# Optimization experiments

Hardware: AMD Instinct MI355X
Metric: run time of the kernel (lower is better)

The kernel has to match this reference:

```python
import jax, jax.numpy as jnp
import numpy as np

N_NODES = 50000
N_EDGES = 800000
HID = 128
EDGE_FEAT = 4
NUM_G = 20
R_MIN, R_MAX = 0.0, 100.0  # r_max = 10.0**2


def _mlp2(x, w1, b1, w2, b2, act_last):
    y = jax.nn.relu(x @ w1 + b1)
    y = y @ w2 + b2
    return jax.nn.relu(y) if act_last else y


def _linear_init(key, fan_in, fan_out):
    kw, kb = jax.random.split(key)
    lim = 1.0 / np.sqrt(fan_in)
    w = jax.random.uniform(kw, (fan_in, fan_out), jnp.float32, -lim, lim)
    b = jax.random.uniform(kb, (fan_out,), jnp.float32, -lim, lim)
    return w, b


def setup_inputs():
    key = jax.random.key(0)
    ks = jax.random.split(key, 16)
    src = jax.random.randint(ks[0], (N_EDGES,), 0, N_NODES)
    dst = jax.random.randint(ks[1], (N_EDGES,), 0, N_NODES)
    edge_feat = jax.random.normal(ks[2], (N_EDGES, EDGE_FEAT), jnp.float32)
    h = jax.random.normal(ks[3], (N_NODES, HID), jnp.float32)
    x = jax.random.normal(ks[4], (N_NODES, 3), jnp.float32)
    ein = 2 * HID + EDGE_FEAT + NUM_G
    ew1, eb1 = _linear_init(ks[5], ein, HID)
    ew2, eb2 = _linear_init(ks[6], HID, HID)
    infw, infb = _linear_init(ks[7], HID, 1)
    xw1, xb1 = _linear_init(ks[8], HID, HID)
    xw2, xb2 = _linear_init(ks[9], HID, 1)
    nw1, nb1 = _linear_init(ks[10], 2 * HID, HID)
    nw2, nb2 = _linear_init(ks[11], HID, HID)
    return {"src": src, "dst": dst, "edge_feat": edge_feat, "h": h, "x": x,
            "ew1": ew1, "eb1": eb1, "ew2": ew2, "eb2": eb2,
            "infw": infw, "infb": infb,
            "xw1": xw1, "xb1": xb1, "xw2": xw2, "xb2": xb2,
            "nw1": nw1, "nb1": nb1, "nw2": nw2, "nb2": nb2}


def reference(src, dst, edge_feat, h, x,
              ew1, eb1, ew2, eb2, infw, infb,
              xw1, xb1, xw2, xb2, nw1, nb1, nw2, nb2):
    n_nodes = h.shape[0]
    rel_x = x[dst] - x[src]                      # [E, 3]
    r = jnp.sum(rel_x * rel_x, -1, keepdims=True)  # [E, 1]
    # GaussianSmearing expansion
    offsets = jnp.linspace(R_MIN, R_MAX, NUM_G)
    coeff = -0.5 / (offsets[1] - offsets[0]) ** 2
    r_feat = jnp.exp(coeff * (r - offsets) ** 2)  # [E, NUM_G]
    # edge message MLP (act_last=True)
    cat = jnp.concatenate([edge_feat, r_feat, h[dst], h[src]], axis=-1)
    mij = _mlp2(cat, ew1, eb1, ew2, eb2, act_last=True)  # [E, HID]
    eij = jax.nn.sigmoid(mij @ infw + infb)              # [E, 1]
    mi = jax.ops.segment_sum(mij * eij, dst, num_segments=n_nodes)  # [N, HID]
    h_new = h + _mlp2(jnp.concatenate([mi, h], -1), nw1, nb1, nw2, nb2, act_last=False)
    # coordinate update: (xi - xj) == rel_x
    x_scale = _mlp2(mij, xw1, xb1, xw2, xb2, act_last=False)  # [E, 1]
    delta_x = jax.ops.segment_sum(rel_x * x_scale, dst, num_segments=n_nodes)
    x_new = x + delta_x
    return h_new, x_new
```

## Files before the change

### kernel.cpp

```cpp
#include <hip/hip_runtime.h>

#define HID 128
#define NNODES 50000
#define NEDGES 800000

typedef __attribute__((ext_vector_type(8))) short short8;
typedef __attribute__((ext_vector_type(4))) float f32x4;

union U8 { short8 v; unsigned short u[8]; };

__device__ __forceinline__ unsigned short f2b(float f) {
  unsigned int u = __float_as_uint(f);
  u += 0x7FFFu + ((u >> 16) & 1u);
  return (unsigned short)(u >> 16);
}

__device__ __forceinline__ unsigned int pk2(float a, float b) {
  unsigned int ua = __float_as_uint(a);
  ua += 0x7FFFu + ((ua >> 16) & 1u);
  unsigned int ub = __float_as_uint(b);
  ub += 0x7FFFu + ((ub >> 16) & 1u);
  return (ua >> 16) | (ub & 0xFFFF0000u);
}

// ... 13 lines not shown

__global__ __launch_bounds__(256) void pack_kernel(
    const float* __restrict__ ew1, const float* __restrict__ ew2,
    const float* __restrict__ xw1, const float* __restrict__ nw1,
    const float* __restrict__ nw2, unsigned short* __restrict__ ws) {
  int i = blockIdx.x * 256 + threadIdx.x;
  const float* w; int base, ksrc;
  if (i < 36864)       { w = ew1; base = 0;      ksrc = 280; }
  else if (i < 53248)  { w = ew2; base = 36864;  ksrc = 128; }
  else if (i < 69632)  { w = xw1; base = 53248;  ksrc = 128; }
  else if (i < 102400) { w = nw1; base = 69632;  ksrc = 256; }
  else if (i < 118784) { w = nw2; base = 102400; ksrc = 128; }
  else return;
  int li = i - base;
  int j = li & 7, t = li >> 3;
  int col = t & 127, kg = t >> 7;
  int k = kg * 8 + j;
  float v = (k < ksrc) ? w[k * 128 + col] : 0.0f;
  ws[i] = f2b(v);
}

__global__ __launch_bounds__(256) void hpack_kernel(
    const float* __restrict__ h, unsigned short* __restrict__ hB) {
  int i = blockIdx.x * 256 + threadIdx.x;
  const float4* p = reinterpret_cast<const float4*>(h + (size_t)i * 8);
  float4 a = p[0], b = p[1];
  uint4 u;
  u.x = pk2(a.x, a.y); u.y = pk2(a.z, a.w);
  u.z = pk2(b.x, b.y); u.w = pk2(b.z, b.w);
  *reinterpret_cast<uint4*>(hB + (size_t)i * 8) = u;
}

template<int MODE>
__global__ __launch_bounds__(256, 4) void edge_kernel(
    const int* __restrict__ src, const int* __restrict__ dst,
    const float* __restrict__ ef, const float* __restrict__ h,
    const float* __restrict__ x,
    const float* __restrict__ eb1, const float* __restrict__ eb2,
    const float* __restrict__ infw, const float* __restrict__ infb,
    const float* __restrict__ xb1, const float* __restrict__ xw2,
    const float* __restrict__ xb2,
    const short8* __restrict__ W1p, const short8* __restrict__ W2p,
    const short8* __restrict__ XW1p,
    const unsigned short* __restrict__ hB,
    float* __restrict__ miF, unsigned short* __restrict__ miB,
    float* __restrict__ dx) {
  __shared__ __align__(16) char catB[64 * 576];
  __shared__ int dL[64], sL[64];
  __shared__ float relL[64][3];
  __shared__ float ppart[4][64];
  __shared__ float eijL[64];

  const int tid = threadIdx.x;
  const int e0 = blockIdx.x * 64;
  const int lane = tid & 63, w = tid >> 6;
  const int lr = lane & 15, lg = lane >> 4;
  const int l7 = lr & 7, l3 = lr & 3;
  const int colb = w*32 + lr;

  {
    int row = tid >> 2, sub = tid & 3;
    int e = e0 + row;
    int s = src[e], d = dst[e];
    if (sub == 0) { sL[row] = s; dL[row] = d; }
    float rx = x[3*d+0] - x[3*s+0];
    float ry = x[3*d+1] - x[3*s+1];
    float rz = x[3*d+2] - x[3*s+2];
    if (sub == 1) { relL[row][0] = rx; relL[row][1] = ry; relL[row][2] = rz; }
    float r = rx*rx + ry*ry + rz*rz;
    const float step = 100.0f / 19.0f;
    const float co = -0.5f / (step * step);
    float v6[6];
    if (sub == 0) {
      const float4 efv = reinterpret_cast<const float4*>(ef)[e];
      v6[0]=efv.x; v6[1]=efv.y; v6[2]=efv.z; v6[3]=efv.w;
      float t1 = r - step;
      v6[4] = __expf(co * r * r);
      v6[5] = __expf(co * t1 * t1);
    } else {
      #pragma unroll
      for (int q = 0; q < 6; ++q) {
        float g = (float)(sub*6 - 4 + q) * step;
        float t = r - g;
        v6[q] = __expf(co * t * t);
      }
    }
    #pragma unroll
    for (int q = 0; q < 3; ++q) {
      int c = sub*6 + q*2;
      int chunk = (c>>3) ^ (row&7);
      *reinterpret_cast<unsigned int*>(catB + row*576 + (chunk<<4) + ((c&7)<<1)) = pk2h(v6[q*2], v6[q*2+1]);
    }
    if (sub == 3) {
      U8 z;
      #pragma unroll
      for (int j = 0; j < 8; ++j) z.u[j] = 0;
      *reinterpret_cast<short8*>(catB + row*576 + ((32 + (3 ^ (row&3)))<<4)) = z.v;
    }
  }

  #pragma unroll
  for (int it = 0; it < 8; ++it) {
    int i = tid + it*256;
    int row = i >> 5, c = i & 31;
    int node = (c < 16) ? dst[e0+row] : src[e0+row];
    int chunk = 3 + c;
    int sw = (chunk < 32) ? (chunk ^ (row&7)) : (32 + ((chunk&3) ^ (row&3)));
    if (MODE == 2) {
      short8 u = *reinterpret_cast<const short8*>(hB + (size_t)node*128 + (c&15)*8);
      *reinterpret_cast<short8*>(catB + row*576 + (sw<<4)) = u;
    } else {
      const float4* hp = reinterpret_cast<const float4*>(h + (size_t)node*128 + (c&15)*8);
      float4 a = hp[0], b = hp[1];
      uint4 u;
      u.x = pk2(a.x, a.y); u.y = pk2(a.z, a.w);
      u.z = pk2(b.x, b.y); u.w = pk2(b.z, b.w);
      *reinterpret_cast<uint4*>(catB + row*576 + (sw<<4)) = u;
    }
  }

  short8 p00 = W1p[(0*4+lg)*128 + colb], p01 = W1p[(0*4+lg)*128 + colb + 16];
  short8 p10 = W1p[(1*4+lg)*128 + colb], p11 = W1p[(1*4+lg)*128 + colb + 16];
  __syncthreads();

  f32x4 acc[4][2];
  #pragma unroll
  for (int t = 0; t < 4; ++t) { acc[t][0] = (f32x4)0.0f; acc[t][1] = (f32x4)0.0f; }
  #pragma unroll
  for (int kt = 0; kt < 9; ++kt) {
    int ch = (kt < 8) ? ((kt*4+lg) ^ l7) : (32 + (lg ^ l3));
    short8 a0 = *reinterpret_cast<const short8*>(catB + (0*16+lr)*576 + (ch<<4));
    short8 a1 = *reinterpret_cast<const short8*>(catB + (1*16+lr)*576 + (ch<<4));
    short8 a2 = *reinterpret_cast<const short8*>(catB + (2*16+lr)*576 + (ch<<4));
    short8 a3 = *reinterpret_cast<const short8*>(catB + (3*16+lr)*576 + (ch<<4));
    short8 b0, b1;
    if (kt == 0)      { b0 = p00; b1 = p01; }
    else if (kt == 1) { b0 = p10; b1 = p11; }
    else              { b0 = W1p[(kt*4+lg)*128 + colb]; b1 = W1p[(kt*4+lg)*128 + colb + 16]; }
    acc[0][0] = __builtin_amdgcn_mfma_f32_16x16x32_bf16(b0, a0, acc[0][0], 0, 0, 0);
    acc[0][1] = __builtin_amdgcn_mfma_f32_16x16x32_bf16(b1, a0, acc[0][1], 0, 0, 0);
    acc[1][0] = __builtin_amdgcn_mfma_f32_16x16x32_bf16(b0, a1, acc[1][0], 0, 0, 0);
    acc[1][1] = __builtin_amdgcn_mfma_f32_16x16x32_bf16(b1, a1, acc[1][1], 0, 0, 0);
    acc[2][0] = __builtin_amdgcn_mfma_f32_16x16x32_bf16(b0, a2, acc[2][0], 0, 0, 0);
    acc[2][1] = __builtin_amdgcn_mfma_f32_16x16x32_bf16(b1, a2, acc[2][1], 0, 0, 0);
    acc[3][0] = __builtin_amdgcn_mfma_f32_16x16x32_bf16(b0, a3, acc[3][0], 0, 0, 0);
    acc[3][1] = __builtin_amdgcn_mfma_f32_16x16x32_bf16(b1, a3, acc[3][1], 0, 0, 0);
  }
  __syncthreads();

  {
    const int c00 = w*32 + lg*4, c01 = c00 + 16;
    float4 be0 = *reinterpret_cast<const float4*>(eb1 + c00);
    float4 be1 = *reinterpret_cast<const float4*>(eb1 + c01);
    #pragma unroll
    for (int t = 0; t < 4; ++t) {
      int row = t*16 + lr;
      char* rowB = catB + row*576;
      #pragma unroll
      for (int j = 0; j < 2; ++j) {
        const float4 be = j ? be1 : be0;
        int c0 = j ? c01 : c00;
        float v0 = fmaxf(acc[t][j][0] + be.x, 0.f);
        float v1 = fmaxf(acc[t][j][1] + be.y, 0.f);
        float v2 = fmaxf(acc[t][j][2] + be.z, 0.f);
        float v3 = fmaxf(acc[t][j][3] + be.w, 0.f);
        uint2 pv; pv.x = pk2h(v0, v1); pv.y = pk2h(v2, v3);
        int chunk = (c0>>3) ^ (row&7);
        *reinterpret_cast<uint2*>(rowB + (chunk<<4) + ((c0&7)<<1)) = pv;
      }
    }
  }
  __syncthreads();

  f32x4 acc2[4][2];
  #pragma unroll
  for (int t = 0; t < 4; ++t) { acc2[t][0] = (f32x4)0.0f; acc2[t][1] = (f32x4)0.0f; }
  #pragma unroll
  for (int kt = 0; kt < 4; ++kt) {
    int ch = (kt*4+lg) ^ l7;
    short8 a0 = *reinterpret_cast<const short8*>(catB + (0*16+lr)*576 + (ch<<4));
    short8 a1 = *reinterpret_cast<const short8*>(catB + (1*16+lr)*576 + (ch<<4));
    short8 a2 = *reinterpret_cast<const short8*>(catB + (2*16+lr)*576 + (ch<<4));
    short8 a3 = *reinterpret_cast<const short8*>(catB + (3*16+lr)*576 + (ch<<4));
    short8 b0 = W2p[(kt*4+lg)*128 + colb];
    short8 b1 = W2p[(kt*4+lg)*128 + colb + 16];
    acc2[0][0] = __builtin_amdgcn_mfma_f32_16x16x32_bf16(b0, a0, acc2[0][0], 0, 0, 0);
    acc2[0][1] = __builtin_amdgcn_mfma_f32_16x16x32_bf16(b1, a0, acc2[0][1], 0, 0, 0);
    acc2[1][0] = __builtin_amdgcn_mfma_f32_16x16x32_bf16(b0, a1, acc2[1][0], 0, 0, 0);
    acc2[1][1] = __builtin_amdgcn_mfma_f32_16x16x32_bf16(b1, a1, acc2[1][1], 0, 0, 0);
    acc2[2][0] = __builtin_amdgcn_mfma_f32_16x16x32_bf16(b0, a2, acc2[2][0], 0, 0, 0);
    acc2[2][1] = __builtin_amdgcn_mfma_f32_16x16x32_bf16(b1, a2, acc2[2][1], 0, 0, 0);
    acc2[3][0] = __builtin_amdgcn_mfma_f32_16x16x32_bf16(b0, a3, acc2[3][0], 0, 0, 0);
    acc2[3][1] = __builtin_amdgcn_mfma_f32_16x16x32_bf16(b1, a3, acc2[3][1], 0, 0, 0);
  }
  float pl[4];
  {
    const int c00 = w*32 + lg*4, c01 = c00 + 16;
    float4 be0 = *reinterpret_cast<const float4*>(eb2 + c00);
    float4 be1 = *reinterpret_cast<const float4*>(eb2 + c01);
    float4 iw0 = *reinterpret_cast<const float4*>(infw + c00);
    float4 iw1 = *reinterpret_cast<const float4*>(infw + c01);
    #pragma unroll
    for (int t = 0; t < 4; ++t) {
      int row = t*16 + lr;
      char* rowB = catB + row*576;
      pl[t] = 0.f;
      #pragma unroll
      for (int j = 0; j < 2; ++j) {
        const float4 be = j ? be1 : be0;
        const float4 iw = j ? iw1 : iw0;
        int c0 = j ? c01 : c00;
        float v0 = fmaxf(acc2[t][j][0] + be.x, 0.f);
        float v1 = fmaxf(acc2[t][j][1] + be.y, 0.f);
        float v2 = fmaxf(acc2[t][j][2] + be.z, 0.f);
        float v3 = fmaxf(acc2[t][j][3] + be.w, 0.f);
        acc2[t][j][0] = v0; acc2[t][j][1] = v1; acc2[t][j][2] = v2; acc2[t][j][3] = v3;
        pl[t] += v0*iw.x + v1*iw.y + v2*iw.z + v3*iw.w;
        uint2 pv; pv.x = pk2h(v0, v1); pv.y = pk2h(v2, v3);
        int chunk = 16 + ((c0>>3) ^ (row&7));
        *reinterpret_cast<uint2*>(rowB + (chunk<<4) + ((c0&7)<<1)) = pv;
      }
    }
    #pragma unroll
    for (int t = 0; t < 4; ++t) {
      pl[t] += __shfl_xor(pl[t], 16, 64);
      pl[t] += __shfl_xor(pl[t], 32, 64);
    }
    if (lane < 16) {
      #pragma unroll
      for (int t = 0; t < 4; ++t) ppart[w][t*16 + lane] = pl[t];
    }
  }
  __syncthreads();

  if (lane < 16) {
    int row2 = w*16 + lane;
    float s2 = ppart[0][row2] + ppart[1][row2] + ppart[2][row2] + ppart[3][row2] + infb[0];
    eijL[row2] = 1.f / (1.f + __expf(-s2));
  }
  __syncthreads();

  if (MODE >= 1) {
    const int c00 = w*32 + lg*4, c01 = c00 + 16;
    #pragma unroll
    for (int t = 0; t < 4; ++t) {
      int row = t*16 + lr;
      float e = eijL[row];
      char* rowB = catB + row*576;
      #pragma unroll
      for (int j = 0; j < 2; ++j) {
        int c0 = j ? c01 : c00;
        uint2 pv;
        pv.x = pk2h(acc2[t][j][0]*e, acc2[t][j][1]*e);
        pv.y = pk2h(acc2[t][j][2]*e, acc2[t][j][3]*e);
        *reinterpret_cast<uint2*>(rowB + (stage_chunk(c0, row)<<4) + ((c0&7)<<1)) = pv;
      }
    }
  } else {
    const int c00 = w*32 + lg*4, c01 = c00 + 16;
    #pragma unroll
    for (int t = 0; t < 4; ++t) {
      int row = t*16 + lr;
      int d = dL[row];
      float e = eijL[row];
      float* fp = miF + (size_t)d*128;
      #pragma unroll
      for (int j = 0; j < 2; ++j) {
        int c0 = j ? c01 : c00;
        #pragma unroll
        for (int rg = 0; rg < 4; ++rg) atomicAdd(fp + c0 + rg, acc2[t][j][rg]*e);
      }
    }
  }
  __syncthreads();

  if (MODE >= 1) {
    #pragma unroll
    for (int t = 0; t < 4; ++t)
      #pragma unroll
      for (int rg = 0; rg < 4; ++rg) {
        int row = t*16 + lg*4 + rg;
        int d = dL[row];
        int col0 = w*32 + lr*2;
        unsigned int val = *reinterpret_cast<const unsigned int*>(
            catB + row*576 + (stage_chunk(col0, row)<<4) + ((col0&7)<<1));
        if (val) atomicPkAddBf16(miB + (size_t)d*128 + col0, val);
      }
  }

  f32x4 acc3[4][2];
  #pragma unroll
  for (int t = 0; t < 4; ++t) { acc3[t][0] = (f32x4)0.0f; acc3[t][1] = (f32x4)0.0f; }
  #pragma unroll
  for (int kt = 0; kt < 4; ++kt) {
    int ch = 16 + ((kt*4+lg) ^ l7);
    short8 a0 = *reinterpret_cast<const short8*>(catB + (0*16+lr)*576 + (ch<<4));
    short8 a1 = *reinterpret_cast<const short8*>(catB + (1*16+lr)*576 + (ch<<4));
    short8 a2 = *reinterpret_cast<const short8*>(catB + (2*16+lr)*576 + (ch<<4));
    short8 a3 = *reinterpret_cast<const short8*>(catB + (3*16+lr)*576 + (ch<<4));
    short8 b0 = XW1p[(kt*4+lg)*128 + colb];
    short8 b1 = XW1p[(kt*4+lg)*128 + colb + 16];
    acc3[0][0] = __builtin_amdgcn_mfma_f32_16x16x32_bf16(b0, a0, acc3[0][0], 0, 0, 0);
    acc3[0][1] = __builtin_amdgcn_mfma_f32_16x16x32_bf16(b1, a0, acc3[0][1], 0, 0, 0);
    acc3[1][0] = __builtin_amdgcn_mfma_f32_16x16x32_bf16(b0, a1, acc3[1][0], 0, 0, 0);
    acc3[1][1] = __builtin_amdgcn_mfma_f32_16x16x32_bf16(b1, a1, acc3[1][1], 0, 0, 0);
    acc3[2][0] = __builtin_amdgcn_mfma_f32_16x16x32_bf16(b0, a2, acc3[2][0], 0, 0, 0);
    acc3[2][1] = __builtin_amdgcn_mfma_f32_16x16x32_bf16(b1, a2, acc3[2][1], 0, 0, 0);
    acc3[3][0] = __builtin_amdgcn_mfma_f32_16x16x32_bf16(b0, a3, acc3[3][0], 0, 0, 0);
    acc3[3][1] = __builtin_amdgcn_mfma_f32_16x16x32_bf16(b1, a3, acc3[3][1], 0, 0, 0);
  }

  {
    const int c00 = w*32 + lg*4, c01 = c00 + 16;
    float4 bx0 = *reinterpret_cast<const float4*>(xb1 + c00);
    float4 bx1 = *reinterpret_cast<const float4*>(xb1 + c01);
    float4 xw0 = *reinterpret_cast<const float4*>(xw2 + c00);
    float4 xw1v = *reinterpret_cast<const float4*>(xw2 + c01);
    float ql[4];
    #pragma unroll
    for (int t = 0; t < 4; ++t) {
      ql[t] = 0.f;
      #pragma unroll
      for (int j = 0; j < 2; ++j) {
        const float4 bx = j ? bx1 : bx0;
        const float4 xw = j ? xw1v : xw0;
        ql[t] += fmaxf(acc3[t][j][0] + bx.x, 0.f) * xw.x
               + fmaxf(acc3[t][j][1] + bx.y, 0.f) * xw.y
               + fmaxf(acc3[t][j][2] + bx.z, 0.f) * xw.z
               + fmaxf(acc3[t][j][3] + bx.w, 0.f) * xw.w;
      }
      ql[t] += __shfl_xor(ql[t], 16, 64);
      ql[t] += __shfl_xor(ql[t], 32, 64);
    }
    if (lane < 16) {
      #pragma unroll
      for (int t = 0; t < 4; ++t) ppart[w][t*16 + lane] = ql[t];
    }
  }
  __syncthreads();

  if (tid < 192) {
    int row = tid / 3, c = tid - row*3;
    float q = ppart[0][row] + ppart[1][row] + ppart[2][row] + ppart[3][row] + xb2[0];
    atomicAdd(dx + dL[row]*3 + c, relL[row][c] * q);
  }
}

template<int MODE>
__global__ __launch_bounds__(256) void node_kernel(
    const float* __restrict__ h, const float* __restrict__ x,
    const float* __restrict__ nb1, const float* __restrict__ nb2,
    const short8* __restrict__ NW1p, const short8* __restrict__ NW2p,
    const unsigned short* __restrict__ miB,
    const unsigned short* __restrict__ hB,
    float* __restrict__ out) {
  __shared__ __align__(16) char c2B[64 * 512];
  __shared__ __align__(16) char y3B[64 * 256];
  const int tid = threadIdx.x;
  const int n0 = blockIdx.x * 64;
  const float* mi = out;

  for (int i = tid; i < 64*32; i += 256) {
    int row = i >> 5, c = i & 31;
    int node = n0 + row;
    U8 u;
    if (node < NNODES) {
      if (c < 16 && MODE >= 1) {
        u.v = *reinterpret_cast<const short8*>(miB + (size_t)node*128 + c*8);
      } else if (c >= 16 && MODE == 2) {
        u.v = *reinterpret_cast<const short8*>(hB + (size_t)node*128 + (c-16)*8);
      } else {
        const float4* p = (c < 16)
          ? reinterpret_cast<const float4*>(mi + (size_t)node*128 + c*8)
          : reinterpret_cast<const float4*>(h + (size_t)node*128 + (c-16)*8);
        float4 a = p[0], b = p[1];
        uint4 uu;
// ... 92 lines not shown
  const float* infb = (const float*)d_in[10];
  const float* xw1  = (const float*)d_in[11];
  const float* xb1  = (const float*)d_in[12];
  const float* xw2  = (const float*)d_in[13];
  const float* xb2  = (const float*)d_in[14];
  const float* nw1  = (const float*)d_in[15];
  const float* nb1  = (const float*)d_in[16];
  const float* nw2  = (const float*)d_in[17];
  const float* nb2  = (const float*)d_in[18];

  float* out = (float*)d_out;
  float* miF = out;
  float* dxp = out + NNODES*HID;
  unsigned short* wsp = (unsigned short*)d_ws;
  unsigned short* miB = wsp + 118784;
  unsigned short* hBp = miB + (size_t)NNODES*HID;

  const size_t MIN = (size_t)NNODES*HID;
  size_t need1 = (118784u + MIN) * 2u;
  size_t need2 = (118784u + 2u*MIN) * 2u;
  int mode = (ws_size >= need2) ? 2 : (ws_size >= need1 ? 1 : 0);

  if (mode >= 1) {
    hipMemsetAsync(miB, 0, MIN*2, stream);
    hipMemsetAsync(dxp, 0, (size_t)NNODES*3*4, stream);
  } else {
    hipMemsetAsync(d_out, 0, (size_t)out_size * sizeof(float), stream);
  }

  pack_kernel<<<464, 256, 0, stream>>>(ew1, ew2, xw1, nw1, nw2, wsp);
  if (mode == 2) hpack_kernel<<<(NNODES*HID)/(256*8), 256, 0, stream>>>(h, hBp);

  if (mode == 2) {
    edge_kernel<2><<<NEDGES/64, 256, 0, stream>>>(
        src, dst, ef, h, x, eb1, eb2, infw, infb, xb1, xw2, xb2,
        (const short8*)wsp, (const short8*)(wsp + 36864), (const short8*)(wsp + 53248),
        hBp, miF, miB, dxp);
    node_kernel<2><<<(NNODES + 63)/64, 256, 0, stream>>>(
        h, x, nb1, nb2,
        (const short8*)(wsp + 69632), (const short8*)(wsp + 102400), miB, hBp, out);
  } else if (mode == 1) {
    edge_kernel<1><<<NEDGES/64, 256, 0, stream>>>(
        src, dst, ef, h, x, eb1, eb2, infw, infb, xb1, xw2, xb2,
        (const short8*)wsp, (const short8*)(wsp + 36864), (const short8*)(wsp + 53248),
        hBp, miF, miB, dxp);
    node_kernel<1><<<(NNODES + 63)/64, 256, 0, stream>>>(
        h, x, nb1, nb2,
        (const short8*)(wsp + 69632), (const short8*)(wsp + 102400), miB, hBp, out);
  } else {
    edge_kernel<0><<<NEDGES/64, 256, 0, stream>>>(
        src, dst, ef, h, x, eb1, eb2, infw, infb, xb1, xw2, xb2,
        (const short8*)wsp, (const short8*)(wsp + 36864), (const short8*)(wsp + 53248),
        hBp, miF, miB, dxp);
    node_kernel<0><<<(NNODES + 63)/64, 256, 0, stream>>>(
        h, x, nb1, nb2,
        (const short8*)(wsp + 69632), (const short8*)(wsp + 102400), miB, hBp, out);
  }
}
```

Before: 314.4 us.

## Split edge kernel work across 8 waves with 16 output columns each

Measured after the change: 458.5 us. 1.46x slower.

```diff
diff --git a/kernel.cpp b/kernel.cpp
--- a/kernel.cpp
+++ b/kernel.cpp
@@ -69,7 +69,7 @@
 }
 
 template<int MODE>
-__global__ __launch_bounds__(256, 4) void edge_kernel(
+__global__ __launch_bounds__(512, 8) void edge_kernel(
     const int* __restrict__ src, const int* __restrict__ dst,
     const float* __restrict__ ef, const float* __restrict__ h,
     const float* __restrict__ x,
@@ -85,7 +85,7 @@
   __shared__ __align__(16) char catB[64 * 576];
   __shared__ int dL[64], sL[64];
   __shared__ float relL[64][3];
-  __shared__ float ppart[4][64];
+  __shared__ float ppart[8][64];
   __shared__ float eijL[64];
 
   const int tid = threadIdx.x;
@@ -93,10 +93,11 @@
   const int lane = tid & 63, w = tid >> 6;
   const int lr = lane & 15, lg = lane >> 4;
   const int l7 = lr & 7, l3 = lr & 3;
-  const int colb = w*32 + lr;
+  const int colb = w*16 + lr;
+  const int c00 = w*16 + lg*4;
 
   {
-    int row = tid >> 2, sub = tid & 3;
+    int row = tid >> 3, sub = tid & 7;
     int e = e0 + row;
     int s = src[e], d = dst[e];
     if (sub == 0) { sL[row] = s; dL[row] = d; }
@@ -107,28 +108,24 @@
     float r = rx*rx + ry*ry + rz*rz;
     const float step = 100.0f / 19.0f;
     const float co = -0.5f / (step * step);
-    float v6[6];
-    if (sub == 0) {
-      const float4 efv = reinterpret_cast<const float4*>(ef)[e];
-      v6[0]=efv.x; v6[1]=efv.y; v6[2]=efv.z; v6[3]=efv.w;
-      float t1 = r - step;
-      v6[4] = __expf(co * r * r);
-      v6[5] = __expf(co * t1 * t1);
-    } else {
-      #pragma unroll
-      for (int q = 0; q < 6; ++q) {
-        float g = (float)(sub*6 - 4 + q) * step;
-        float t = r - g;
-        v6[q] = __expf(co * t * t);
+    if (sub < 6) {
+      float v4[4];
+      if (sub == 0) {
+        const float4 efv = reinterpret_cast<const float4*>(ef)[e];
+        v4[0]=efv.x; v4[1]=efv.y; v4[2]=efv.z; v4[3]=efv.w;
+      } else {
+        #pragma unroll
+        for (int q = 0; q < 4; ++q) {
+          float g = (float)(sub*4 - 4 + q) * step;
+          float t = r - g;
+          v4[q] = __expf(co * t * t);
+        }
       }
-    }
-    #pragma unroll
-    for (int q = 0; q < 3; ++q) {
-      int c = sub*6 + q*2;
+      int c = sub*4;
       int chunk = (c>>3) ^ (row&7);
-      *reinterpret_cast<unsigned int*>(catB + row*576 + (chunk<<4) + ((c&7)<<1)) = pk2h(v6[q*2], v6[q*2+1]);
-    }
-    if (sub == 3) {
+      uint2 pv; pv.x = pk2h(v4[0], v4[1]); pv.y = pk2h(v4[2], v4[3]);
+      *reinterpret_cast<uint2*>(catB + row*576 + (chunk<<4) + ((c&7)<<1)) = pv;
+    } else if (sub == 6) {
       U8 z;
       #pragma unroll
       for (int j = 0; j < 8; ++j) z.u[j] = 0;
@@ -137,8 +134,8 @@
   }
 
   #pragma unroll
-  for (int it = 0; it < 8; ++it) {
-    int i = tid + it*256;
+  for (int it = 0; it < 4; ++it) {
+    int i = tid + it*512;
     int row = i >> 5, c = i & 31;
     int node = (c < 16) ? dst[e0+row] : src[e0+row];
     int chunk = 3 + c;
@@ -156,13 +153,13 @@
     }
   }
 
-  short8 p00 = W1p[(0*4+lg)*128 + colb], p01 = W1p[(0*4+lg)*128 + colb + 16];
-  short8 p10 = W1p[(1*4+lg)*128 + colb], p11 = W1p[(1*4+lg)*128 + colb + 16];
-  __syncthreads();
-
-  f32x4 acc[4][2];
-  #pragma unroll
-  for (int t = 0; t < 4; ++t) { acc[t][0] = (f32x4)0.0f; acc[t][1] = (f32x4)0.0f; }
+  short8 p00 = W1p[(0*4+lg)*128 + colb];
+  short8 p10 = W1p[(1*4+lg)*128 + colb];
+  __syncthreads();
+
+  f32x4 acc[4];
+  #pragma unroll
+  for (int t = 0; t < 4; ++t) acc[t] = (f32x4)0.0f;
   #pragma unroll
   for (int kt = 0; kt < 9; ++kt) {
     int ch = (kt < 8) ? ((kt*4+lg) ^ l7) : (32 + (lg ^ l3));
@@ -170,48 +167,33 @@
     short8 a1 = *reinterpret_cast<const short8*>(catB + (1*16+lr)*576 + (ch<<4));
     short8 a2 = *reinterpret_cast<const short8*>(catB + (2*16+lr)*576 + (ch<<4));
     short8 a3 = *reinterpret_cast<const short8*>(catB + (3*16+lr)*576 + (ch<<4));
-    short8 b0, b1;
-    if (kt == 0)      { b0 = p00; b1 = p01; }
-    else if (kt == 1) { b0 = p10; b1 = p11; }
-    else              { b0 = W1p[(kt*4+lg)*128 + colb]; b1 = W1p[(kt*4+lg)*128 + colb + 16]; }
-    acc[0][0] = __builtin_amdgcn_mfma_f32_16x16x32_bf16(b0, a0, acc[0][0], 0, 0, 0);
-    acc[0][1] = __builtin_amdgcn_mfma_f32_16x16x32_bf16(b1, a0, acc[0][1], 0, 0, 0);
-    acc[1][0] = __builtin_amdgcn_mfma_f32_16x16x32_bf16(b0, a1, acc[1][0], 0, 0, 0);
-    acc[1][1] = __builtin_amdgcn_mfma_f32_16x16x32_bf16(b1, a1, acc[1][1], 0, 0, 0);
-    acc[2][0] = __builtin_amdgcn_mfma_f32_16x16x32_bf16(b0, a2, acc[2][0], 0, 0, 0);
-    acc[2][1] = __builtin_amdgcn_mfma_f32_16x16x32_bf16(b1, a2, acc[2][1], 0, 0, 0);
-    acc[3][0] = __builtin_amdgcn_mfma_f32_16x16x32_bf16(b0, a3, acc[3][0], 0, 0, 0);
-    acc[3][1] = __builtin_amdgcn_mfma_f32_16x16x32_bf16(b1, a3, acc[3][1], 0, 0, 0);
+    short8 b0 = (kt == 0) ? p00 : (kt == 1) ? p10 : W1p[(kt*4+lg)*128 + colb];
+    acc[0] = __builtin_amdgcn_mfma_f32_16x16x32_bf16(b0, a0, acc[0], 0, 0, 0);
+    acc[1] = __builtin_amdgcn_mfma_f32_16x16x32_bf16(b0, a1, acc[1], 0, 0, 0);
+    acc[2] = __builtin_amdgcn_mfma_f32_16x16x32_bf16(b0, a2, acc[2], 0, 0, 0);
+    acc[3] = __builtin_amdgcn_mfma_f32_16x16x32_bf16(b0, a3, acc[3], 0, 0, 0);
   }
   __syncthreads();
 
   {
-    const int c00 = w*32 + lg*4, c01 = c00 + 16;
-    float4 be0 = *reinterpret_cast<const float4*>(eb1 + c00);
-    float4 be1 = *reinterpret_cast<const float4*>(eb1 + c01);
+    float4 be = *reinterpret_cast<const float4*>(eb1 + c00);
     #pragma unroll
     for (int t = 0; t < 4; ++t) {
       int row = t*16 + lr;
-      char* rowB = catB + row*576;
-      #pragma unroll
-      for (int j = 0; j < 2; ++j) {
-        const float4 be = j ? be1 : be0;
-        int c0 = j ? c01 : c00;
-        float v0 = fmaxf(acc[t][j][0] + be.x, 0.f);
-        float v1 = fmaxf(acc[t][j][1] + be.y, 0.f);
-        float v2 = fmaxf(acc[t][j][2] + be.z, 0.f);
-        float v3 = fmaxf(acc[t][j][3] + be.w, 0.f);
-        uint2 pv; pv.x = pk2h(v0, v1); pv.y = pk2h(v2, v3);
-        int chunk = (c0>>3) ^ (row&7);
-        *reinterpret_cast<uint2*>(rowB + (chunk<<4) + ((c0&7)<<1)) = pv;
-      }
-    }
-  }
-  __syncthreads();
-
-  f32x4 acc2[4][2];
-  #pragma unroll
-  for (int t = 0; t < 4; ++t) { acc2[t][0] = (f32x4)0.0f; acc2[t][1] = (f32x4)0.0f; }
+      float v0 = fmaxf(acc[t][0] + be.x, 0.f);
+      float v1 = fmaxf(acc[t][1] + be.y, 0.f);
+      float v2 = fmaxf(acc[t][2] + be.z, 0.f);
+      float v3 = fmaxf(acc[t][3] + be.w, 0.f);
+      uint2 pv; pv.x = pk2h(v0, v1); pv.y = pk2h(v2, v3);
+      int chunk = (c00>>3) ^ (row&7);
+      *reinterpret_cast<uint2*>(catB + row*576 + (chunk<<4) + ((c00&7)<<1)) = pv;
+    }
+  }
+  __syncthreads();
+
+  f32x4 acc2[4];
+  #pragma unroll
+  for (int t = 0; t < 4; ++t) acc2[t] = (f32x4)0.0f;
   #pragma unroll
   for (int kt = 0; kt < 4; ++kt) {
     int ch = (kt*4+lg) ^ l7;
@@ -220,43 +202,27 @@
     short8 a2 = *reinterpret_cast<const short8*>(catB + (2*16+lr)*576 + (ch<<4));
     short8 a3 = *reinterpret_cast<const short8*>(catB + (3*16+lr)*576 + (ch<<4));
     short8 b0 = W2p[(kt*4+lg)*128 + colb];
-    short8 b1 = W2p[(kt*4+lg)*128 + colb + 16];
-    acc2[0][0] = __builtin_amdgcn_mfma_f32_16x16x32_bf16(b0, a0, acc2[0][0], 0, 0, 0);
-    acc2[0][1] = __builtin_amdgcn_mfma_f32_16x16x32_bf16(b1, a0, acc2[0][1], 0, 0, 0);
-    acc2[1][0] = __builtin_amdgcn_mfma_f32_16x16x32_bf16(b0, a1, acc2[1][0], 0, 0, 0);
-    acc2[1][1] = __builtin_amdgcn_mfma_f32_16x16x32_bf16(b1, a1, acc2[1][1], 0, 0, 0);
-    acc2[2][0] = __builtin_amdgcn_mfma_f32_16x16x32_bf16(b0, a2, acc2[2][0], 0, 0, 0);
-    acc2[2][1] = __builtin_amdgcn_mfma_f32_16x16x32_bf16(b1, a2, acc2[2][1], 0, 0, 0);
-    acc2[3][0] = __builtin_amdgcn_mfma_f32_16x16x32_bf16(b0, a3, acc2[3][0], 0, 0, 0);
-    acc2[3][1] = __builtin_amdgcn_mfma_f32_16x16x32_bf16(b1, a3, acc2[3][1], 0, 0, 0);
-  }
-  float pl[4];
+    acc2[0] = __builtin_amdgcn_mfma_f32_16x16x32_bf16(b0, a0, acc2[0], 0, 0, 0);
+    acc2[1] = __builtin_amdgcn_mfma_f32_16x16x32_bf16(b0, a1, acc2[1], 0, 0, 0);
+    acc2[2] = __builtin_amdgcn_mfma_f32_16x16x32_bf16(b0, a2, acc2[2], 0, 0, 0);
+    acc2[3] = __builtin_amdgcn_mfma_f32_16x16x32_bf16(b0, a3, acc2[3], 0, 0, 0);
+  }
   {
-    const int c00 = w*32 + lg*4, c01 = c00 + 16;
-    float4 be0 = *reinterpret_cast<const float4*>(eb2 + c00);
-    float4 be1 = *reinterpret_cast<const float4*>(eb2 + c01);
-    float4 iw0 = *reinterpret_cast<const float4*>(infw + c00);
-    float4 iw1 = *reinterpret_cast<const float4*>(infw + c01);
+    float4 be = *reinterpret_cast<const float4*>(eb2 + c00);
+    float4 iw = *reinterpret_cast<const float4*>(infw + c00);
+    float pl[4];
     #pragma unroll
     for (int t = 0; t < 4; ++t) {
       int row = t*16 + lr;
-      char* rowB = catB + row*576;
-      pl[t] = 0.f;
-      #pragma unroll
-      for (int j = 0; j < 2; ++j) {
-        const float4 be = j ? be1 : be0;
-        const float4 iw = j ? iw1 : iw0;
-        int c0 = j ? c01 : c00;
-        float v0 = fmaxf(acc2[t][j][0] + be.x, 0.f);
-        float v1 = fmaxf(acc2[t][j][1] + be.y, 0.f);
-        float v2 = fmaxf(acc2[t][j][2] + be.z, 0.f);
-        float v3 = fmaxf(acc2[t][j][3] + be.w, 0.f);
-        acc2[t][j][0] = v0; acc2[t][j][1] = v1; acc2[t][j][2] = v2; acc2[t][j][3] = v3;
-        pl[t] += v0*iw.x + v1*iw.y + v2*iw.z + v3*iw.w;
-        uint2 pv; pv.x = pk2h(v0, v1); pv.y = pk2h(v2, v3);
-        int chunk = 16 + ((c0>>3) ^ (row&7));
-        *reinterpret_cast<uint2*>(rowB + (chunk<<4) + ((c0&7)<<1)) = pv;
-      }
+      float v0 = fmaxf(acc2[t][0] + be.x, 0.f);
+      float v1 = fmaxf(acc2[t][1] + be.y, 0.f);
+      float v2 = fmaxf(acc2[t][2] + be.z, 0.f);
+      float v3 = fmaxf(acc2[t][3] + be.w, 0.f);
+      acc2[t][0]=v0; acc2[t][1]=v1; acc2[t][2]=v2; acc2[t][3]=v3;
+      pl[t] = v0*iw.x + v1*iw.y + v2*iw.z + v3*iw.w;
+      uint2 pv; pv.x = pk2h(v0, v1); pv.y = pk2h(v2, v3);
+      int chunk = 16 + ((c00>>3) ^ (row&7));
+      *reinterpret_cast<uint2*>(catB + row*576 + (chunk<<4) + ((c00&7)<<1)) = pv;
     }
     #pragma unroll
     for (int t = 0; t < 4; ++t) {
@@ -270,31 +236,25 @@
   }
   __syncthreads();
 
-  if (lane < 16) {
-    int row2 = w*16 + lane;
-    float s2 = ppart[0][row2] + ppart[1][row2] + ppart[2][row2] + ppart[3][row2] + infb[0];
-    eijL[row2] = 1.f / (1.f + __expf(-s2));
+  if (tid < 64) {
+    float s2 = infb[0];
+    #pragma unroll
+    for (int ww = 0; ww < 8; ++ww) s2 += ppart[ww][tid];
+    eijL[tid] = 1.f / (1.f + __expf(-s2));
   }
   __syncthreads();
 
   if (MODE >= 1) {
-    const int c00 = w*32 + lg*4, c01 = c00 + 16;
     #pragma unroll
     for (int t = 0; t < 4; ++t) {
       int row = t*16 + lr;
       float e = eijL[row];
-      char* rowB = catB + row*576;
-      #pragma unroll
-      for (int j = 0; j < 2; ++j) {
-        int c0 = j ? c01 : c00;
-        uint2 pv;
-        pv.x = pk2h(acc2[t][j][0]*e, acc2[t][j][1]*e);
-        pv.y = pk2h(acc2[t][j][2]*e, acc2[t][j][3]*e);
-        *reinterpret_cast<uint2*>(rowB + (stage_chunk(c0, row)<<4) + ((c0&7)<<1)) = pv;
-      }
+      uint2 pv;
+      pv.x = pk2h(acc2[t][0]*e, acc2[t][1]*e);
+      pv.y = pk2h(acc2[t][2]*e, acc2[t][3]*e);
+      *reinterpret_cast<uint2*>(catB + row*576 + (stage_chunk(c00, row)<<4) + ((c00&7)<<1)) = pv;
     }
   } else {
-    const int c00 = w*32 + lg*4, c01 = c00 + 16;
     #pragma unroll
     for (int t = 0; t < 4; ++t) {
       int row = t*16 + lr;
@@ -302,32 +262,27 @@
       float e = eijL[row];
       float* fp = miF + (size_t)d*128;
       #pragma unroll
-      for (int j = 0; j < 2; ++j) {
-        int c0 = j ? c01 : c00;
-        #pragma unroll
-        for (int rg = 0; rg < 4; ++rg) atomicAdd(fp + c0 + rg, acc2[t][j][rg]*e);
-      }
+      for (int rg = 0; rg < 4; ++rg) atomicAdd(fp + c00 + rg, acc2[t][rg]*e);
     }
   }
   __syncthreads();
 
   if (MODE >= 1) {
-    #pragma unroll
-    for (int t = 0; t < 4; ++t)
-      #pragma unroll
-      for (int rg = 0; rg < 4; ++rg) {
-        int row = t*16 + lg*4 + rg;
-        int d = dL[row];
-        int col0 = w*32 + lr*2;
-        unsigned int val = *reinterpret_cast<const unsigned int*>(
-            catB + row*576 + (stage_chunk(col0, row)<<4) + ((col0&7)<<1));
-        if (val) atomicPkAddBf16(miB + (size_t)d*128 + col0, val);
-      }
-  }
-
-  f32x4 acc3[4][2];
-  #pragma unroll
-  for (int t = 0; t < 4; ++t) { acc3[t][0] = (f32x4)0.0f; acc3[t][1] = (f32x4)0.0f; }
+    int col0 = w*16 + (lr & 7)*2;
+    int rsel = lg*2 + (lr >> 3);
+    #pragma unroll
+    for (int t2 = 0; t2 < 8; ++t2) {
+      int row = t2*8 + rsel;
+      int d = dL[row];
+      unsigned int val = *reinterpret_cast<const unsigned int*>(
+          catB + row*576 + (stage_chunk(col0, row)<<4) + ((col0&7)<<1));
+      if (val) atomicPkAddBf16(miB + (size_t)d*128 + col0, val);
+    }
+  }
+
+  f32x4 acc3[4];
+  #pragma unroll
+  for (int t = 0; t < 4; ++t) acc3[t] = (f32x4)0.0f;
   #pragma unroll
   for (int kt = 0; kt < 4; ++kt) {
     int ch = 16 + ((kt*4+lg) ^ l7);
@@ -336,36 +291,21 @@
     short8 a2 = *reinterpret_cast<const short8*>(catB + (2*16+lr)*576 + (ch<<4));
     short8 a3 = *reinterpret_cast<const short8*>(catB + (3*16+lr)*576 + (ch<<4));
     short8 b0 = XW1p[(kt*4+lg)*128 + colb];
-    short8 b1 = XW1p[(kt*4+lg)*128 + colb + 16];
-    acc3[0][0] = __builtin_amdgcn_mfma_f32_16x16x32_bf16(b0, a0, acc3[0][0], 0, 0, 0);
-    acc3[0][1] = __builtin_amdgcn_mfma_f32_16x16x32_bf16(b1, a0, acc3[0][1], 0, 0, 0);
-    acc3[1][0] = __builtin_amdgcn_mfma_f32_16x16x32_bf16(b0, a1, acc3[1][0], 0, 0, 0);
-    acc3[1][1] = __builtin_amdgcn_mfma_f32_16x16x32_bf16(b1, a1, acc3[1][1], 0, 0, 0);
-    acc3[2][0] = __builtin_amdgcn_mfma_f32_16x16x32_bf16(b0, a2, acc3[2][0], 0, 0, 0);
-    acc3[2][1] = __builtin_amdgcn_mfma_f32_16x16x32_bf16(b1, a2, acc3[2][1], 0, 0, 0);
-    acc3[3][0] = __builtin_amdgcn_mfma_f32_16x16x32_bf16(b0, a3, acc3[3][0], 0, 0, 0);
-    acc3[3][1] = __builtin_amdgcn_mfma_f32_16x16x32_bf16(b1, a3, acc3[3][1], 0, 0, 0);
-  }
-
+    acc3[0] = __builtin_amdgcn_mfma_f32_16x16x32_bf16(b0, a0, acc3[0], 0, 0, 0);
+    acc3[1] = __builtin_amdgcn_mfma_f32_16x16x32_bf16(b0, a1, acc3[1], 0, 0, 0);
+    acc3[2] = __builtin_amdgcn_mfma_f32_16x16x32_bf16(b0, a2, acc3[2], 0, 0, 0);
+    acc3[3] = __builtin_amdgcn_mfma_f32_16x16x32_bf16(b0, a3, acc3[3], 0, 0, 0);
+  }
   {
-    const int c00 = w*32 + lg*4, c01 = c00 + 16;
-    float4 bx0 = *reinterpret_cast<const float4*>(xb1 + c00);
-    float4 bx1 = *reinterpret_cast<const float4*>(xb1 + c01);
-    float4 xw0 = *reinterpret_cast<const float4*>(xw2 + c00);
-    float4 xw1v = *reinterpret_cast<const float4*>(xw2 + c01);
+    float4 bx = *reinterpret_cast<const float4*>(xb1 + c00);
+    float4 xw = *reinterpret_cast<const float4*>(xw2 + c00);
     float ql[4];
     #pragma unroll
     for (int t = 0; t < 4; ++t) {
-      ql[t] = 0.f;
-      #pragma unroll
-      for (int j = 0; j < 2; ++j) {
-        const float4 bx = j ? bx1 : bx0;
-        const float4 xw = j ? xw1v : xw0;
-        ql[t] += fmaxf(acc3[t][j][0] + bx.x, 0.f) * xw.x
-               + fmaxf(acc3[t][j][1] + bx.y, 0.f) * xw.y
-               + fmaxf(acc3[t][j][2] + bx.z, 0.f) * xw.z
-               + fmaxf(acc3[t][j][3] + bx.w, 0.f) * xw.w;
-      }
+      ql[t] = fmaxf(acc3[t][0] + bx.x, 0.f) * xw.x
+            + fmaxf(acc3[t][1] + bx.y, 0.f) * xw.y
+            + fmaxf(acc3[t][2] + bx.z, 0.f) * xw.z
+            + fmaxf(acc3[t][3] + bx.w, 0.f) * xw.w;
       ql[t] += __shfl_xor(ql[t], 16, 64);
       ql[t] += __shfl_xor(ql[t], 32, 64);
     }
@@ -378,7 +318,9 @@
 
   if (tid < 192) {
     int row = tid / 3, c = tid - row*3;
-    float q = ppart[0][row] + ppart[1][row] + ppart[2][row] + ppart[3][row] + xb2[0];
+    float q = xb2[0];
+    #pragma unroll
+    for (int ww = 0; ww < 8; ++ww) q += ppart[ww][row];
     atomicAdd(dx + dL[row]*3 + c, relL[row][c] * q);
   }
 }
@@ -537,7 +479,7 @@
   if (mode == 2) hpack_kernel<<<(NNODES*HID)/(256*8), 256, 0, stream>>>(h, hBp);
 
   if (mode == 2) {
-    edge_kernel<2><<<NEDGES/64, 256, 0, stream>>>(
+    edge_kernel<2><<<NEDGES/64, 512, 0, stream>>>(
         src, dst, ef, h, x, eb1, eb2, infw, infb, xb1, xw2, xb2,
         (const short8*)wsp, (const short8*)(wsp + 36864), (const short8*)(wsp + 53248),
         hBp, miF, miB, dxp);
@@ -545,7 +487,7 @@
         h, x, nb1, nb2,
         (const short8*)(wsp + 69632), (const short8*)(wsp + 102400), miB, hBp, out);
   } else if (mode == 1) {
-    edge_kernel<1><<<NEDGES/64, 256, 0, stream>>>(
+    edge_kernel<1><<<NEDGES/64, 512, 0, stream>>>(
         src, dst, ef, h, x, eb1, eb2, infw, infb, xb1, xw2, xb2,
         (const short8*)wsp, (const short8*)(wsp + 36864), (const short8*)(wsp + 53248),
         hBp, miF, miB, dxp);
@@ -553,7 +495,7 @@
         h, x, nb1, nb2,
         (const short8*)(wsp + 69632), (const short8*)(wsp + 102400), miB, hBp, out);
   } else {
-    edge_kernel<0><<<NEDGES/64, 256, 0, stream>>>(
+    edge_kernel<0><<<NEDGES/64, 512, 0, stream>>>(
         src, dst, ef, h, x, eb1, eb2, infw, infb, xb1, xw2, xb2,
         (const short8*)wsp, (const short8*)(wsp + 36864), (const short8*)(wsp + 53248),
         hBp, miF, miB, dxp);
```

## Split edge kernel work across 8 waves with 2x4 row/column wave tiling

Applied to the files above, without the earlier changes.

New measurement: 313.1 us (median of 2 runs). About the same (-0.4%).

```diff
diff --git a/kernel.cpp b/kernel.cpp
--- a/kernel.cpp
+++ b/kernel.cpp
@@ -69,7 +69,7 @@
 }
 
 template<int MODE>
-__global__ __launch_bounds__(256, 4) void edge_kernel(
+__global__ __launch_bounds__(512, 8) void edge_kernel(
     const int* __restrict__ src, const int* __restrict__ dst,
     const float* __restrict__ ef, const float* __restrict__ h,
     const float* __restrict__ x,
@@ -85,18 +85,21 @@
   __shared__ __align__(16) char catB[64 * 576];
   __shared__ int dL[64], sL[64];
   __shared__ float relL[64][3];
-  __shared__ float ppart[4][64];
+  __shared__ float ppart[8][64];
   __shared__ float eijL[64];
 
   const int tid = threadIdx.x;
   const int e0 = blockIdx.x * 64;
   const int lane = tid & 63, w = tid >> 6;
+  const int wm = w >> 2, wn = w & 3;
   const int lr = lane & 15, lg = lane >> 4;
   const int l7 = lr & 7, l3 = lr & 3;
-  const int colb = w*32 + lr;
+  const int colb = wn*32 + lr;
+  const int c00 = wn*32 + lg*4, c01 = c00 + 16;
+  const int rbase = wm*32;
 
   {
-    int row = tid >> 2, sub = tid & 3;
+    int row = tid >> 3, sub = tid & 7;
     int e = e0 + row;
     int s = src[e], d = dst[e];
     if (sub == 0) { sL[row] = s; dL[row] = d; }
@@ -107,28 +110,24 @@
     float r = rx*rx + ry*ry + rz*rz;
     const float step = 100.0f / 19.0f;
     const float co = -0.5f / (step * step);
-    float v6[6];
-    if (sub == 0) {
-      const float4 efv = reinterpret_cast<const float4*>(ef)[e];
-      v6[0]=efv.x; v6[1]=efv.y; v6[2]=efv.z; v6[3]=efv.w;
-      float t1 = r - step;
-      v6[4] = __expf(co * r * r);
-      v6[5] = __expf(co * t1 * t1);
-    } else {
-      #pragma unroll
-      for (int q = 0; q < 6; ++q) {
-        float g = (float)(sub*6 - 4 + q) * step;
-        float t = r - g;
-        v6[q] = __expf(co * t * t);
-      }
-    }
-    #pragma unroll
-    for (int q = 0; q < 3; ++q) {
-      int c = sub*6 + q*2;
+    if (sub < 6) {
+      float v4[4];
+      if (sub == 0) {
+        const float4 efv = reinterpret_cast<const float4*>(ef)[e];
+        v4[0]=efv.x; v4[1]=efv.y; v4[2]=efv.z; v4[3]=efv.w;
+      } else {
+        #pragma unroll
+        for (int q = 0; q < 4; ++q) {
+          float g = (float)(sub*4 - 4 + q) * step;
+          float t = r - g;
+          v4[q] = __expf(co * t * t);
+        }
+      }
+      int c = sub*4;
       int chunk = (c>>3) ^ (row&7);
-      *reinterpret_cast<unsigned int*>(catB + row*576 + (chunk<<4) + ((c&7)<<1)) = pk2h(v6[q*2], v6[q*2+1]);
-    }
-    if (sub == 3) {
+      uint2 pv; pv.x = pk2h(v4[0], v4[1]); pv.y = pk2h(v4[2], v4[3]);
+      *reinterpret_cast<uint2*>(catB + row*576 + (chunk<<4) + ((c&7)<<1)) = pv;
+    } else if (sub == 6) {
       U8 z;
       #pragma unroll
       for (int j = 0; j < 8; ++j) z.u[j] = 0;
@@ -137,8 +136,8 @@
   }
 
   #pragma unroll
-  for (int it = 0; it < 8; ++it) {
-    int i = tid + it*256;
+  for (int it = 0; it < 4; ++it) {
+    int i = tid + it*512;
     int row = i >> 5, c = i & 31;
     int node = (c < 16) ? dst[e0+row] : src[e0+row];
     int chunk = 3 + c;
@@ -160,16 +159,14 @@
   short8 p10 = W1p[(1*4+lg)*128 + colb], p11 = W1p[(1*4+lg)*128 + colb + 16];
   __syncthreads();
 
-  f32x4 acc[4][2];
-  #pragma unroll
-  for (int t = 0; t < 4; ++t) { acc[t][0] = (f32x4)0.0f; acc[t][1] = (f32x4)0.0f; }
+  f32x4 acc[2][2];
+  #pragma unroll
+  for (int t = 0; t < 2; ++t) { acc[t][0] = (f32x4)0.0f; acc[t][1] = (f32x4)0.0f; }
   #pragma unroll
   for (int kt = 0; kt < 9; ++kt) {
     int ch = (kt < 8) ? ((kt*4+lg) ^ l7) : (32 + (lg ^ l3));
-    short8 a0 = *reinterpret_cast<const short8*>(catB + (0*16+lr)*576 + (ch<<4));
-    short8 a1 = *reinterpret_cast<const short8*>(catB + (1*16+lr)*576 + (ch<<4));
-    short8 a2 = *reinterpret_cast<const short8*>(catB + (2*16+lr)*576 + (ch<<4));
-    short8 a3 = *reinterpret_cast<const short8*>(catB + (3*16+lr)*576 + (ch<<4));
+    short8 a0 = *reinterpret_cast<const short8*>(catB + (rbase + 0*16 + lr)*576 + (ch<<4));
+    short8 a1 = *reinterpret_cast<const short8*>(catB + (rbase + 1*16 + lr)*576 + (ch<<4));
     short8 b0, b1;
     if (kt == 0)      { b0 = p00; b1 = p01; }
     else if (kt == 1) { b0 = p10; b1 = p11; }
@@ -178,20 +175,15 @@
     acc[0][1] = __builtin_amdgcn_mfma_f32_16x16x32_bf16(b1, a0, acc[0][1], 0, 0, 0);
     acc[1][0] = __builtin_amdgcn_mfma_f32_16x16x32_bf16(b0, a1, acc[1][0], 0, 0, 0);
     acc[1][1] = __builtin_amdgcn_mfma_f32_16x16x32_bf16(b1, a1, acc[1][1], 0, 0, 0);
-    acc[2][0] = __builtin_amdgcn_mfma_f32_16x16x32_bf16(b0, a2, acc[2][0], 0, 0, 0);
-    acc[2][1] = __builtin_amdgcn_mfma_f32_16x16x32_bf16(b1, a2, acc[2][1], 0, 0, 0);
-    acc[3][0] = __builtin_amdgcn_mfma_f32_16x16x32_bf16(b0, a3, acc[3][0], 0, 0, 0);
-    acc[3][1] = __builtin_amdgcn_mfma_f32_16x16x32_bf16(b1, a3, acc[3][1], 0, 0, 0);
   }
   __syncthreads();
 
   {
-    const int c00 = w*32 + lg*4, c01 = c00 + 16;
     float4 be0 = *reinterpret_cast<const float4*>(eb1 + c00);
     float4 be1 = *reinterpret_cast<const float4*>(eb1 + c01);
     #pragma unroll
-    for (int t = 0; t < 4; ++t) {
-      int row = t*16 + lr;
+    for (int t = 0; t < 2; ++t) {
+      int row = rbase + t*16 + lr;
       char* rowB = catB + row*576;
       #pragma unroll
       for (int j = 0; j < 2; ++j) {
@@ -209,37 +201,30 @@
   }
   __syncthreads();
 
-  f32x4 acc2[4][2];
-  #pragma unroll
-  for (int t = 0; t < 4; ++t) { acc2[t][0] = (f32x4)0.0f; acc2[t][1] = (f32x4)0.0f; }
+  f32x4 acc2[2][2];
+  #pragma unroll
+  for (int t = 0; t < 2; ++t) { acc2[t][0] = (f32x4)0.0f; acc2[t][1] = (f32x4)0.0f; }
   #pragma unroll
   for (int kt = 0; kt < 4; ++kt) {
     int ch = (kt*4+lg) ^ l7;
-    short8 a0 = *reinterpret_cast<const short8*>(catB + (0*16+lr)*576 + (ch<<4));
-    short8 a1 = *reinterpret_cast<const short8*>(catB + (1*16+lr)*576 + (ch<<4));
-    short8 a2 = *reinterpret_cast<const short8*>(catB + (2*16+lr)*576 + (ch<<4));
-    short8 a3 = *reinterpret_cast<const short8*>(catB + (3*16+lr)*576 + (ch<<4));
+    short8 a0 = *reinterpret_cast<const short8*>(catB + (rbase + 0*16 + lr)*576 + (ch<<4));
+    short8 a1 = *reinterpret_cast<const short8*>(catB + (rbase + 1*16 + lr)*576 + (ch<<4));
     short8 b0 = W2p[(kt*4+lg)*128 + colb];
     short8 b1 = W2p[(kt*4+lg)*128 + colb + 16];
     acc2[0][0] = __builtin_amdgcn_mfma_f32_16x16x32_bf16(b0, a0, acc2[0][0], 0, 0, 0);
     acc2[0][1] = __builtin_amdgcn_mfma_f32_16x16x32_bf16(b1, a0, acc2[0][1], 0, 0, 0);
     acc2[1][0] = __builtin_amdgcn_mfma_f32_16x16x32_bf16(b0, a1, acc2[1][0], 0, 0, 0);
     acc2[1][1] = __builtin_amdgcn_mfma_f32_16x16x32_bf16(b1, a1, acc2[1][1], 0, 0, 0);
-    acc2[2][0] = __builtin_amdgcn_mfma_f32_16x16x32_bf16(b0, a2, acc2[2][0], 0, 0, 0);
-    acc2[2][1] = __builtin_amdgcn_mfma_f32_16x16x32_bf16(b1, a2, acc2[2][1], 0, 0, 0);
-    acc2[3][0] = __builtin_amdgcn_mfma_f32_16x16x32_bf16(b0, a3, acc2[3][0], 0, 0, 0);
-    acc2[3][1] = __builtin_amdgcn_mfma_f32_16x16x32_bf16(b1, a3, acc2[3][1], 0, 0, 0);
-  }
-  float pl[4];
+  }
   {
-    const int c00 = w*32 + lg*4, c01 = c00 + 16;
     float4 be0 = *reinterpret_cast<const float4*>(eb2 + c00);
     float4 be1 = *reinterpret_cast<const float4*>(eb2 + c01);
     float4 iw0 = *reinterpret_cast<const float4*>(infw + c00);
     float4 iw1 = *reinterpret_cast<const float4*>(infw + c01);
-    #pragma unroll
-    for (int t = 0; t < 4; ++t) {
-      int row = t*16 + lr;
+    float pl[2];
+    #pragma unroll
+    for (int t = 0; t < 2; ++t) {
+      int row = rbase + t*16 + lr;
       char* rowB = catB + row*576;
       pl[t] = 0.f;
       #pragma unroll
@@ -251,7 +236,7 @@
         float v1 = fmaxf(acc2[t][j][1] + be.y, 0.f);
         float v2 = fmaxf(acc2[t][j][2] + be.z, 0.f);
         float v3 = fmaxf(acc2[t][j][3] + be.w, 0.f);
-        acc2[t][j][0] = v0; acc2[t][j][1] = v1; acc2[t][j][2] = v2; acc2[t][j][3] = v3;
+        acc2[t][j][0]=v0; acc2[t][j][1]=v1; acc2[t][j][2]=v2; acc2[t][j][3]=v3;
         pl[t] += v0*iw.x + v1*iw.y + v2*iw.z + v3*iw.w;
         uint2 pv; pv.x = pk2h(v0, v1); pv.y = pk2h(v2, v3);
         int chunk = 16 + ((c0>>3) ^ (row&7));
@@ -259,29 +244,29 @@
       }
     }
     #pragma unroll
-    for (int t = 0; t < 4; ++t) {
+    for (int t = 0; t < 2; ++t) {
       pl[t] += __shfl_xor(pl[t], 16, 64);
       pl[t] += __shfl_xor(pl[t], 32, 64);
     }
     if (lane < 16) {
       #pragma unroll
-      for (int t = 0; t < 4; ++t) ppart[w][t*16 + lane] = pl[t];
-    }
-  }
-  __syncthreads();
-
-  if (lane < 16) {
-    int row2 = w*16 + lane;
-    float s2 = ppart[0][row2] + ppart[1][row2] + ppart[2][row2] + ppart[3][row2] + infb[0];
-    eijL[row2] = 1.f / (1.f + __expf(-s2));
+      for (int t = 0; t < 2; ++t) ppart[w][rbase + t*16 + lane] = pl[t];
+    }
+  }
+  __syncthreads();
+
+  if (tid < 64) {
+    int wmr = tid >> 5;
+    float s2 = infb[0] + ppart[wmr*4+0][tid] + ppart[wmr*4+1][tid]
+                       + ppart[wmr*4+2][tid] + ppart[wmr*4+3][tid];
+    eijL[tid] = 1.f / (1.f + __expf(-s2));
   }
   __syncthreads();
 
   if (MODE >= 1) {
-    const int c00 = w*32 + lg*4, c01 = c00 + 16;
-    #pragma unroll
-    for (int t = 0; t < 4; ++t) {
-      int row = t*16 + lr;
+    #pragma unroll
+    for (int t = 0; t < 2; ++t) {
+      int row = rbase + t*16 + lr;
       float e = eijL[row];
       char* rowB = catB + row*576;
       #pragma unroll
@@ -294,10 +279,9 @@
       }
     }
   } else {
-    const int c00 = w*32 + lg*4, c01 = c00 + 16;
-    #pragma unroll
-    for (int t = 0; t < 4; ++t) {
-      int row = t*16 + lr;
+    #pragma unroll
+    for (int t = 0; t < 2; ++t) {
+      int row = rbase + t*16 + lr;
       int d = dL[row];
       float e = eijL[row];
       float* fp = miF + (size_t)d*128;
@@ -312,50 +296,40 @@
   __syncthreads();
 
   if (MODE >= 1) {
-    #pragma unroll
-    for (int t = 0; t < 4; ++t)
-      #pragma unroll
-      for (int rg = 0; rg < 4; ++rg) {
-        int row = t*16 + lg*4 + rg;
-        int d = dL[row];
-        int col0 = w*32 + lr*2;
-        unsigned int val = *reinterpret_cast<const unsigned int*>(
-            catB + row*576 + (stage_chunk(col0, row)<<4) + ((col0&7)<<1));
-        if (val) atomicPkAddBf16(miB + (size_t)d*128 + col0, val);
-      }
-  }
-
-  f32x4 acc3[4][2];
-  #pragma unroll
-  for (int t = 0; t < 4; ++t) { acc3[t][0] = (f32x4)0.0f; acc3[t][1] = (f32x4)0.0f; }
+    int col0 = wn*32 + lr*2;
+    #pragma unroll
+    for (int t2 = 0; t2 < 8; ++t2) {
+      int row = rbase + t2*4 + lg;
+      int d = dL[row];
+      unsigned int val = *reinterpret_cast<const unsigned int*>(
+          catB + row*576 + (stage_chunk(col0, row)<<4) + ((col0&7)<<1));
+      if (val) atomicPkAddBf16(miB + (size_t)d*128 + col0, val);
+    }
+  }
+
+  f32x4 acc3[2][2];
+  #pragma unroll
+  for (int t = 0; t < 2; ++t) { acc3[t][0] = (f32x4)0.0f; acc3[t][1] = (f32x4)0.0f; }
   #pragma unroll
   for (int kt = 0; kt < 4; ++kt) {
     int ch = 16 + ((kt*4+lg) ^ l7);
-    short8 a0 = *reinterpret_cast<const short8*>(catB + (0*16+lr)*576 + (ch<<4));
-    short8 a1 = *reinterpret_cast<const short8*>(catB + (1*16+lr)*576 + (ch<<4));
-    short8 a2 = *reinterpret_cast<const short8*>(catB + (2*16+lr)*576 + (ch<<4));
-    short8 a3 = *reinterpret_cast<const short8*>(catB + (3*16+lr)*576 + (ch<<4));
+    short8 a0 = *reinterpret_cast<const short8*>(catB + (rbase + 0*16 + lr)*576 + (ch<<4));
+    short8 a1 = *reinterpret_cast<const short8*>(catB + (rbase + 1*16 + lr)*576 + (ch<<4));
     short8 b0 = XW1p[(kt*4+lg)*128 + colb];
     short8 b1 = XW1p[(kt*4+lg)*128 + colb + 16];
     acc3[0][0] = __builtin_amdgcn_mfma_f32_16x16x32_bf16(b0, a0, acc3[0][0], 0, 0, 0);
     acc3[0][1] = __builtin_amdgcn_mfma_f32_16x16x32_bf16(b1, a0, acc3[0][1], 0, 0, 0);
     acc3[1][0] = __builtin_amdgcn_mfma_f32_16x16x32_bf16(b0, a1, acc3[1][0], 0, 0, 0);
     acc3[1][1] = __builtin_amdgcn_mfma_f32_16x16x32_bf16(b1, a1, acc3[1][1], 0, 0, 0);
-    acc3[2][0] = __builtin_amdgcn_mfma_f32_16x16x32_bf16(b0, a2, acc3[2][0], 0, 0, 0);
-    acc3[2][1] = __builtin_amdgcn_mfma_f32_16x16x32_bf16(b1, a2, acc3[2][1], 0, 0, 0);
-    acc3[3][0] = __builtin_amdgcn_mfma_f32_16x16x32_bf16(b0, a3, acc3[3][0], 0, 0, 0);
-    acc3[3][1] = __builtin_amdgcn_mfma_f32_16x16x32_bf16(b1, a3, acc3[3][1], 0, 0, 0);
-  }
-
+  }
   {
-    const int c00 = w*32 + lg*4, c01 = c00 + 16;
     float4 bx0 = *reinterpret_cast<const float4*>(xb1 + c00);
     float4 bx1 = *reinterpret_cast<const float4*>(xb1 + c01);
     float4 xw0 = *reinterpret_cast<const float4*>(xw2 + c00);
     float4 xw1v = *reinterpret_cast<const float4*>(xw2 + c01);
-    float ql[4];
-    #pragma unroll
-    for (int t = 0; t < 4; ++t) {
+    float ql[2];
+    #pragma unroll
+    for (int t = 0; t < 2; ++t) {
       ql[t] = 0.f;
       #pragma unroll
       for (int j = 0; j < 2; ++j) {
@@ -371,14 +345,16 @@
     }
     if (lane < 16) {
       #pragma unroll
-      for (int t = 0; t < 4; ++t) ppart[w][t*16 + lane] = ql[t];
+      for (int t = 0; t < 2; ++t) ppart[w][rbase + t*16 + lane] = ql[t];
     }
   }
   __syncthreads();
 
   if (tid < 192) {
     int row = tid / 3, c = tid - row*3;
-    float q = ppart[0][row] + ppart[1][row] + ppart[2][row] + ppart[3][row] + xb2[0];
+    int wmr = row >> 5;
+    float q = xb2[0] + ppart[wmr*4+0][row] + ppart[wmr*4+1][row]
+                     + ppart[wmr*4+2][row] + ppart[wmr*4+3][row];
     atomicAdd(dx + dL[row]*3 + c, relL[row][c] * q);
   }
 }
@@ -537,7 +513,7 @@
   if (mode == 2) hpack_kernel<<<(NNODES*HID)/(256*8), 256, 0, stream>>>(h, hBp);
 
   if (mode == 2) {
-    edge_kernel<2><<<NEDGES/64, 256, 0, stream>>>(
+    edge_kernel<2><<<NEDGES/64, 512, 0, stream>>>(
         src, dst, ef, h, x, eb1, eb2, infw, infb, xb1, xw2, xb2,
         (const short8*)wsp, (const short8*)(wsp + 36864), (const short8*)(wsp + 53248),
         hBp, miF, miB, dxp);
@@ -545,7 +521,7 @@
         h, x, nb1, nb2,
         (const short8*)(wsp + 69632), (const short8*)(wsp + 102400), miB, hBp, out);
   } else if (mode == 1) {
-    edge_kernel<1><<<NEDGES/64, 256, 0, stream>>>(
+    edge_kernel<1><<<NEDGES/64, 512, 0, stream>>>(
         src, dst, ef, h, x, eb1, eb2, infw, infb, xb1, xw2, xb2,
         (const short8*)wsp, (const short8*)(wsp + 36864), (const short8*)(wsp + 53248),
         hBp, miF, miB, dxp);
@@ -553,7 +529,7 @@
         h, x, nb1, nb2,
         (const short8*)(wsp + 69632), (const short8*)(wsp + 102400), miB, hBp, out);
   } else {
-    edge_kernel<0><<<NEDGES/64, 256, 0, stream>>>(
+    edge_kernel<0><<<NEDGES/64, 512, 0, stream>>>(
         src, dst, ef, h, x, eb1, eb2, infw, infb, xb1, xw2, xb2,
         (const short8*)wsp, (const short8*)(wsp + 36864), (const short8*)(wsp + 53248),
         hBp, miF, miB, dxp);
```
